# Kernel optimization log

Measured on AMD Instinct MI355X. Metric: run time of the kernel, lower is better.

Reference implementation:

```python
import math
import jax, jax.numpy as jnp
import numpy as np

G = 96       # grid side; N = G*G tokens, one token per grid cell
D = 512      # d_model
R = 2        # radius (Chebyshev)
LN_EPS = 1e-5

# 24 neighbor offsets in the (2R+1)^2 window, excluding (0,0) (self is excluded in the torch code)
_OFF = np.array([(dx, dy) for dx in range(-R, R + 1) for dy in range(-R, R + 1) if not (dx == 0 and dy == 0)], dtype=np.int32)


def _layer_norm(x, g, b):
    m = jnp.mean(x, axis=-1, keepdims=True)
    v = jnp.mean(jnp.square(x - m), axis=-1, keepdims=True)
    return (x - m) * jax.lax.rsqrt(v + LN_EPS) * g + b


def setup_inputs() -> dict:
    key = jax.random.key(0)
    ks = jax.random.split(key, 12)
    N = G * G
    x = jax.random.normal(ks[0], (N, D), jnp.float32)
    gx, gy = jnp.meshgrid(jnp.arange(G), jnp.arange(G), indexing='ij')
    grid = jnp.stack([gx.ravel(), gy.ravel()], axis=-1).astype(jnp.int32)  # [N,2], one token per cell

    def lin(k, din, dout):
        return jax.random.normal(k, (din, dout), jnp.float32) * (1.0 / math.sqrt(din))

    return {
        'x': x, 'grid': grid,
        'Wq': lin(ks[1], D, D), 'bq': jnp.zeros((D,), jnp.float32),
        'Wk': lin(ks[2], D, D), 'bk': jnp.zeros((D,), jnp.float32),
        'Wv': lin(ks[3], D, D), 'bv': jnp.zeros((D,), jnp.float32),
        'Wo': lin(ks[4], D, D), 'bo': jnp.zeros((D,), jnp.float32),
        'g1': jnp.ones((D,), jnp.float32), 'b1': jnp.zeros((D,), jnp.float32),
        'g2': jnp.ones((D,), jnp.float32), 'b2': jnp.zeros((D,), jnp.float32),
        'W1': lin(ks[5], D, 4 * D), 'bf1': jnp.zeros((4 * D,), jnp.float32),
        'W2': lin(ks[6], 4 * D, D), 'bf2': jnp.zeros((D,), jnp.float32),
    }


def reference(x, grid, Wq, bq, Wk, bk, Wv, bv, Wo, bo, g1, b1, g2, b2, W1, bf1, W2, bf2):
    # dropout is identity (eval mode)
    h = _layer_norm(x, g1, b1)
    q = h @ Wq + bq
    k = h @ Wk + bk
    v = h @ Wv + bv

    off = jnp.asarray(_OFF)                      # [K=24, 2]
    nx = grid[:, 0:1] + off[None, :, 0]          # [N, K]
    ny = grid[:, 1:2] + off[None, :, 1]
    valid = (nx >= 0) & (nx < G) & (ny >= 0) & (ny < G)
    idx = jnp.where(valid, nx * G + ny, 0)       # row-major cell -> token index

    k_nbr = k[idx]                               # [N, K, D]
    v_nbr = v[idx]                               # [N, K, D]
    scores = jnp.einsum('nd,nkd->nk', q, k_nbr) / math.sqrt(D)
    neg = jnp.finfo(scores.dtype).min
    scores = jnp.where(valid, scores, neg)
    attn = jax.nn.softmax(scores, axis=-1)       # every token has >=8 valid neighbors for G>R
    out = jnp.einsum('nk,nkd->nd', attn, v_nbr)  # [N, D]

    x = x + out @ Wo + bo
    h2 = _layer_norm(x, g2, b2)
    ffn = jax.nn.gelu(h2 @ W1 + bf1, approximate=False) @ W2 + bf2
    return x + ffn
```

## Files before the change

kernel.cpp:

```cpp
#include <hip/hip_runtime.h>

typedef unsigned short u16;
typedef unsigned int u32;
typedef __bf16 bf16x8 __attribute__((ext_vector_type(8)));
typedef float f32x4 __attribute__((ext_vector_type(4)));

#define GRID_G 96
#define DMODEL 512
#define NTOK (GRID_G * GRID_G)

__device__ __forceinline__ u16 f2bf(float f) {
  u32 u = __builtin_bit_cast(u32, f);
  u += 0x7fffu + ((u >> 16) & 1u);
  return (u16)(u >> 16);
}
__device__ __forceinline__ void unpack8(uint4 u, float* f) {
  f[0] = __builtin_bit_cast(float, u.x << 16);
  f[1] = __builtin_bit_cast(float, u.x & 0xffff0000u);
  f[2] = __builtin_bit_cast(float, u.y << 16);
  f[3] = __builtin_bit_cast(float, u.y & 0xffff0000u);
  f[4] = __builtin_bit_cast(float, u.z << 16);
  f[5] = __builtin_bit_cast(float, u.z & 0xffff0000u);
  f[6] = __builtin_bit_cast(float, u.w << 16);
  f[7] = __builtin_bit_cast(float, u.w & 0xffff0000u);
}
__device__ __forceinline__ float gelu_fast(float x) {
  float y = 0.7978845608f * (x + 0.044715f * x * x * x);
  float a = fabsf(y);
  float e = __expf(-2.0f * a);
  float th = (1.0f - e) / (1.0f + e);
  th = __builtin_copysignf(th, y);
  return 0.5f * x * (1.0f + th);
}

__global__ __launch_bounds__(256) void k_transpose_bf16(
    const float* __restrict__ src, u16* __restrict__ dst, int R, int C) {
  __shared__ float tile[32][33];
  int bx = blockIdx.x * 32, by = blockIdx.y * 32;
  int tx = threadIdx.x & 31, ty = threadIdx.x >> 5;
#pragma unroll
  for (int i = 0; i < 4; ++i) {
    int r = ty + i * 8;
    tile[r][tx] = src[(size_t)(by + r) * C + (bx + tx)];
  }
  __syncthreads();
#pragma unroll
  for (int i = 0; i < 4; ++i) {
    int c = ty + i * 8;
    dst[(size_t)(bx + c) * R + (by + tx)] = f2bf(tile[tx][c]);
  }
}

__global__ __launch_bounds__(256) void k_transpose4(
    const float* __restrict__ s0, const float* __restrict__ s1,
    const float* __restrict__ s2, const float* __restrict__ s3,
    u16* __restrict__ d0, u16* __restrict__ d1,
    u16* __restrict__ d2, u16* __restrict__ d3) {
  __shared__ float tile[32][33];
  const float* src = blockIdx.z == 0 ? s0 : blockIdx.z == 1 ? s1 : blockIdx.z == 2 ? s2 : s3;
  u16* dst = blockIdx.z == 0 ? d0 : blockIdx.z == 1 ? d1 : blockIdx.z == 2 ? d2 : d3;
  int bx = blockIdx.x * 32, by = blockIdx.y * 32;
  int tx = threadIdx.x & 31, ty = threadIdx.x >> 5;
#pragma unroll
  for (int i = 0; i < 4; ++i) {
    int r = ty + i * 8;
    tile[r][tx] = src[(size_t)(by + r) * 512 + (bx + tx)];
  }
  __syncthreads();
#pragma unroll
  for (int i = 0; i < 4; ++i) {
    int c = ty + i * 8;
    dst[(size_t)(bx + c) * 512 + (by + tx)] = f2bf(tile[tx][c]);
  }
}

__global__ __launch_bounds__(256) void k_concat3(
    const float* __restrict__ a, const float* __restrict__ b,
    const float* __restrict__ c, float* __restrict__ o) {
  int i = blockIdx.x * 256 + threadIdx.x;
  if (i < 512) o[i] = a[i];
  else if (i < 1024) o[i] = b[i - 512];
  else o[i] = c[i - 1024];
}

__global__ __launch_bounds__(256) void k_layernorm_bf16(
    const float* __restrict__ x, const float* __restrict__ g,
    const float* __restrict__ b, u16* __restrict__ out) {
  int tid = threadIdx.x, wid = tid >> 6, lane = tid & 63;
  int row = blockIdx.x * 4 + wid;
  const float* xr = x + (size_t)row * DMODEL;
  float4 v0 = *(const float4*)(xr + lane * 4);
  float4 v1 = *(const float4*)(xr + 256 + lane * 4);
  float s = v0.x + v0.y + v0.z + v0.w + v1.x + v1.y + v1.z + v1.w;
  float sq = v0.x * v0.x + v0.y * v0.y + v0.z * v0.z + v0.w * v0.w +
             v1.x * v1.x + v1.y * v1.y + v1.z * v1.z + v1.w * v1.w;
#pragma unroll
  for (int m = 1; m < 64; m <<= 1) {
    s += __shfl_xor(s, m);
    sq += __shfl_xor(sq, m);
  }
  float mean = s * (1.0f / DMODEL);
  float rstd = rsqrtf(sq * (1.0f / DMODEL) - mean * mean + 1e-5f);
  float4 ga = *(const float4*)(g + lane * 4);
  float4 gb = *(const float4*)(g + 256 + lane * 4);
  float4 ba = *(const float4*)(b + lane * 4);
  float4 bb = *(const float4*)(b + 256 + lane * 4);
  ushort4 o0, o1;
  o0.x = f2bf((v0.x - mean) * rstd * ga.x + ba.x);
  o0.y = f2bf((v0.y - mean) * rstd * ga.y + ba.y);
  o0.z = f2bf((v0.z - mean) * rstd * ga.z + ba.z);
  o0.w = f2bf((v0.w - mean) * rstd * ga.w + ba.w);
  o1.x = f2bf((v1.x - mean) * rstd * gb.x + bb.x);
  o1.y = f2bf((v1.y - mean) * rstd * gb.y + bb.y);
  o1.z = f2bf((v1.z - mean) * rstd * gb.z + bb.z);
  o1.w = f2bf((v1.w - mean) * rstd * gb.w + bb.w);
  u16* op = out + (size_t)row * DMODEL;
  *(ushort4*)(op + lane * 4) = o0;
  *(ushort4*)(op + 256 + lane * 4) = o1;
}

__global__ __launch_bounds__(256) void k_attn(
    const u16* __restrict__ q, const u16* __restrict__ kk,
    const u16* __restrict__ vv, const int* __restrict__ gpos,
    u16* __restrict__ out) {
  int tid = threadIdx.x, wid = tid >> 6, lane = tid & 63;
  int n = blockIdx.x * 4 + wid;
  int px = gpos[2 * n], py = gpos[2 * n + 1];
  float qf[8];
  unpack8(*(const uint4*)(q + (size_t)n * DMODEL + lane * 8), qf);
  float sc[24];
  int nid[24];
  bool ok[24];
#pragma unroll
  for (int j = 0; j < 24; ++j) {
    int jj = j < 12 ? j : j + 1;
    int dx = jj / 5 - 2, dy = jj % 5 - 2;
    int nx = px + dx, ny = py + dy;
    bool val = (nx >= 0) && (nx < GRID_G) && (ny >= 0) && (ny < GRID_G);
    int id = val ? nx * GRID_G + ny : 0;
    ok[j] = val;
    nid[j] = id;
    float kf[8];
    unpack8(*(const uint4*)(kk + (size_t)id * DMODEL + lane * 8), kf);
    float p = 0.f;
#pragma unroll
    for (int e = 0; e < 8; ++e) p += qf[e] * kf[e];
#pragma unroll
    for (int m = 1; m < 64; m <<= 1) p += __shfl_xor(p, m);
    sc[j] = p * 0.04419417382415922f;
  }
  float mx = -3.0e38f;
#pragma unroll
  for (int j = 0; j < 24; ++j)
    if (ok[j]) mx = fmaxf(mx, sc[j]);
  float wsum = 0.f, w[24];
#pragma unroll
  for (int j = 0; j < 24; ++j) {
    w[j] = ok[j] ? expf(sc[j] - mx) : 0.f;
    wsum += w[j];
  }
  float inv = 1.0f / wsum;
  float acc[8] = {0, 0, 0, 0, 0, 0, 0, 0};
#pragma unroll
  for (int j = 0; j < 24; ++j) {
    float vf[8];
    unpack8(*(const uint4*)(vv + (size_t)nid[j] * DMODEL + lane * 8), vf);
    float wj = w[j];
#pragma unroll
    for (int e = 0; e < 8; ++e) acc[e] += wj * vf[e];
  }
  uint4 o;
  o.x = (u32)f2bf(acc[0] * inv) | ((u32)f2bf(acc[1] * inv) << 16);
  o.y = (u32)f2bf(acc[2] * inv) | ((u32)f2bf(acc[3] * inv) << 16);
  o.z = (u32)f2bf(acc[4] * inv) | ((u32)f2bf(acc[5] * inv) << 16);
  o.w = (u32)f2bf(acc[6] * inv) | ((u32)f2bf(acc[7] * inv) << 16);
  *(uint4*)(out + (size_t)n * DMODEL + lane * 8) = o;
}

#define BARR { __builtin_amdgcn_s_barrier(); __builtin_amdgcn_sched_barrier(0); }
#define WAIT8 asm volatile("s_waitcnt vmcnt(8)" ::: "memory");
#define WAIT0 asm volatile("s_waitcnt vmcnt(0)" ::: "memory");

template <int EPI>
__global__ __launch_bounds__(256, 2) void k_gemm(
    const u16* __restrict__ A, const u16* __restrict__ Bt,
    const float* __restrict__ bias, const float* __restrict__ res,
    float* __restrict__ outF, u16* __restrict__ outB,
    int M, int N, int K, int tiles_n) {
  __shared__ u16 lds[32768];
  const int t = threadIdx.x, wid = t >> 6, lane = t & 63;
  const int nwg = gridDim.x, bid = blockIdx.x;
  const int l = ((bid & 7) * (nwg >> 3)) + (bid >> 3);
  const int bM = (l / tiles_n) * 128, bN = (l % tiles_n) * 128;
  const int wr = wid >> 1, wc = wid & 1, lr = lane & 15, lg = lane >> 4;

  const int rs = lane >> 3;
  const int cl = (lane & 7) ^ rs;
  const u16* gA[4];
  const u16* gB[4];
  int dstL[4];
#pragma unroll
  for (int j = 0; j < 4; ++j) {
    int r = wid * 32 + j * 8 + rs;
    gA[j] = A + (size_t)(bM + r) * K + cl * 8;
    gB[j] = Bt + (size_t)(bN + r) * K + cl * 8;
    dstL[j] = wid * 2048 + j * 512;
  }

#define STAGE(BUF, KOFF)                                                              \
  {                                                                                   \
    _Pragma("unroll") for (int j = 0; j < 4; ++j) {                                   \
      __builtin_amdgcn_global_load_lds(                                               \
          (const __attribute__((address_space(1))) void*)(gA[j] + (KOFF)),            \
          (__attribute__((address_space(3))) void*)(lds + (BUF)*16384 + dstL[j]),     \
          16, 0, 0);                                                                  \
      __builtin_amdgcn_global_load_lds(                                               \
          (const __attribute__((address_space(1))) void*)(gB[j] + (KOFF)),            \
          (__attribute__((address_space(3))) void*)(lds + (BUF)*16384 + 8192 + dstL[j]), \
          16, 0, 0);                                                                  \
    }                                                                                 \
  }

  const int offA0 = (wr * 64 + lr) * 64 + ((0 + lg) ^ (lr & 7)) * 8;
  const int offA1 = (wr * 64 + lr) * 64 + ((4 + lg) ^ (lr & 7)) * 8;
  const int offB0 = (wc * 64 + lr) * 64 + ((0 + lg) ^ (lr & 7)) * 8;
  const int offB1 = (wc * 64 + lr) * 64 + ((4 + lg) ^ (lr & 7)) * 8;

  f32x4 acc[4][4];
#pragma unroll
  for (int i = 0; i < 4; ++i)
#pragma unroll
    for (int j = 0; j < 4; ++j) acc[i][j] = (f32x4){0.f, 0.f, 0.f, 0.f};

#define COMPUTE(BUF)                                                                  \
  {                                                                                   \
    _Pragma("unroll") for (int ks = 0; ks < 2; ++ks) {                                \
      const int oa = (BUF)*16384 + (ks ? offA1 : offA0);                              \
      const int ob = (BUF)*16384 + 8192 + (ks ? offB1 : offB0);                       \
      bf16x8 af[4], bfr[4];                                                           \
      _Pragma("unroll") for (int mt = 0; mt < 4; ++mt)                                \
          af[mt] = __builtin_bit_cast(bf16x8, *(const uint4*)(lds + oa + mt * 1024)); \
      _Pragma("unroll") for (int nt = 0; nt < 4; ++nt)                                \
          bfr[nt] = __builtin_bit_cast(bf16x8, *(const uint4*)(lds + ob + nt * 1024));\
      _Pragma("unroll") for (int mt = 0; mt < 4; ++mt)                                \
          _Pragma("unroll") for (int nt = 0; nt < 4; ++nt)                            \
              acc[mt][nt] = __builtin_amdgcn_mfma_f32_16x16x32_bf16(                  \
                  af[mt], bfr[nt], acc[mt][nt], 0, 0, 0);                             \
    }                                                                                 \
  }

  const int nk = K >> 6;
  STAGE(0, 0);
  int koff = 64;
  for (int tt = 0; tt < nk; tt += 2) {
    if (tt + 1 < nk) { STAGE(1, koff); WAIT8 } else { WAIT0 }
    BARR;
    COMPUTE(0);
    BARR;
    if (tt + 2 < nk) { STAGE(0, koff + 64); WAIT8 } else { WAIT0 }
    BARR;
    COMPUTE(1);
    BARR;
    koff += 128;
  }
#undef STAGE
#undef COMPUTE

#pragma unroll
  for (int mt = 0; mt < 4; ++mt) {
#pragma unroll
    for (int nt = 0; nt < 4; ++nt) {
      int col = bN + wc * 64 + nt * 16 + lr;
      float bc = bias[col];
      int row0 = bM + wr * 64 + mt * 16 + lg * 4;
#pragma unroll
      for (int r = 0; r < 4; ++r) {
        float val = acc[mt][nt][r] + bc;
        if constexpr (EPI == 1) {
          size_t off = (size_t)(row0 + r) * N + col;
          outF[off] = res[off] + val;
        } else if constexpr (EPI == 2) {
          size_t off = (size_t)(row0 + r) * N + col;
          outB[off] = f2bf(gelu_fast(val));
        } else {
          int seg = col >> 9;
          size_t off = (size_t)seg * ((size_t)NTOK * DMODEL) +
                       (size_t)(row0 + r) * DMODEL + (col & 511);
          outB[off] = f2bf(val);
        }
      }
    }
  }
}

extern "C" void kernel_launch(void* const* d_in, const int* in_sizes, int n_in,
                              void* d_out, int out_size, void* d_ws, size_t ws_size,
                              hipStream_t stream) {
  const float* x = (const float*)d_in[0];
  const int* gpos = (const int*)d_in[1];
  const float* Wq = (const float*)d_in[2];
  const float* bq = (const float*)d_in[3];
  const float* Wk = (const float*)d_in[4];
  const float* bk = (const float*)d_in[5];
  const float* Wv = (const float*)d_in[6];
  const float* bv = (const float*)d_in[7];
  const float* Wo = (const float*)d_in[8];
  const float* bo = (const float*)d_in[9];
  const float* g1 = (const float*)d_in[10];
  const float* b1 = (const float*)d_in[11];
  const float* g2 = (const float*)d_in[12];
  const float* b2 = (const float*)d_in[13];
  const float* W1 = (const float*)d_in[14];
  const float* bf1 = (const float*)d_in[15];
  const float* W2 = (const float*)d_in[16];
  const float* bf2 = (const float*)d_in[17];
  float* out = (float*)d_out;
  char* ws = (char*)d_ws;

  constexpr size_t SZ_W512 = (size_t)512 * 512 * 2;
  constexpr size_t SZ_W2048 = (size_t)512 * 2048 * 2;
  constexpr size_t SZ_ACT = (size_t)NTOK * 512 * 2;

  u16* WQT = (u16*)(ws + 0);
  u16* WKT = (u16*)(ws + SZ_W512);
  u16* WVT = (u16*)(ws + 2 * SZ_W512);
  u16* WOT = (u16*)(ws + 3 * SZ_W512);
  u16* W1T = (u16*)(ws + 4 * SZ_W512);
  u16* W2T = (u16*)(ws + 4 * SZ_W512 + SZ_W2048);
  float* BCAT = (float*)(ws + 4 * SZ_W512 + 2 * SZ_W2048);
  char* actbase = ws + 4 * SZ_W512 + 2 * SZ_W2048 + 6144;
  u16* H = (u16*)(actbase);
  u16* Q = (u16*)(actbase + SZ_ACT);
  u16* KB = (u16*)(actbase + 2 * SZ_ACT);
  u16* VB = (u16*)(actbase + 3 * SZ_ACT);
  u16* H2 = (u16*)(actbase + 4 * SZ_ACT);
  u16* U = (u16*)(actbase);

  k_transpose4<<<dim3(16, 16, 4), 256, 0, stream>>>(Wq, Wk, Wv, Wo, WQT, WKT, WVT, WOT);
  k_transpose_bf16<<<dim3(64, 16), 256, 0, stream>>>(W1, W1T, 512, 2048);
  k_transpose_bf16<<<dim3(16, 64), 256, 0, stream>>>(W2, W2T, 2048, 512);
  k_concat3<<<6, 256, 0, stream>>>(bq, bk, bv, BCAT);

  k_layernorm_bf16<<<NTOK / 4, 256, 0, stream>>>(x, g1, b1, H);

  k_gemm<3><<<864, 256, 0, stream>>>(H, WQT, BCAT, nullptr, nullptr, Q, NTOK, 1536, 512, 12);

  k_attn<<<NTOK / 4, 256, 0, stream>>>(Q, KB, VB, gpos, H);

  k_gemm<1><<<288, 256, 0, stream>>>(H, WOT, bo, x, out, nullptr, NTOK, 512, 512, 4);

  k_layernorm_bf16<<<NTOK / 4, 256, 0, stream>>>(out, g2, b2, H2);

  k_gemm<2><<<1152, 256, 0, stream>>>(H2, W1T, bf1, nullptr, nullptr, U, NTOK, 2048, 512, 16);

  k_gemm<1><<<288, 256, 0, stream>>>(U, W2T, bf2, out, out, nullptr, NTOK, 512, 2048, 4);
}
```

Baseline: 164.9 us.

## Fuse prep kernels and add 256x256 pipelined GEMM for QKV and FFN1

Merges the weight transposes, bias concat and first layernorm into a single prep launch to cut launch overhead. Adds a new 512-thread GEMM with 256x256 tiles, direct global-to-LDS loads, XOR-swizzled LDS, double buffering interleaved with MFMA phases, and XCD-aware block remapping; it is used for the QKV and W1 projections. The rounding helper now uses the native bf16 conversion. The large tiles use 128KB of LDS and yield fewer blocks (216 and 288), which risks poor wave balance across CUs.

```diff
diff --git a/kernel.cpp b/kernel.cpp
--- a/kernel.cpp
+++ b/kernel.cpp
@@ -10,9 +10,7 @@
 #define NTOK (GRID_G * GRID_G)
 
 __device__ __forceinline__ u16 f2bf(float f) {
-  u32 u = __builtin_bit_cast(u32, f);
-  u += 0x7fffu + ((u >> 16) & 1u);
-  return (u16)(u >> 16);
+  return __builtin_bit_cast(u16, (__bf16)f);
 }
 __device__ __forceinline__ void unpack8(uint4 u, float* f) {
   f[0] = __builtin_bit_cast(float, u.x << 16);
@@ -33,54 +31,84 @@
   return 0.5f * x * (1.0f + th);
 }
 
-__global__ __launch_bounds__(256) void k_transpose_bf16(
-    const float* __restrict__ src, u16* __restrict__ dst, int R, int C) {
-  __shared__ float tile[32][33];
-  int bx = blockIdx.x * 32, by = blockIdx.y * 32;
+__device__ __forceinline__ void tr_tile(const float* __restrict__ src,
+                                        u16* __restrict__ dst, int R, int C,
+                                        int bx, int by, float (*tile)[33]) {
   int tx = threadIdx.x & 31, ty = threadIdx.x >> 5;
 #pragma unroll
   for (int i = 0; i < 4; ++i) {
     int r = ty + i * 8;
-    tile[r][tx] = src[(size_t)(by + r) * C + (bx + tx)];
+    tile[r][tx] = src[(size_t)(by * 32 + r) * C + (bx * 32 + tx)];
   }
   __syncthreads();
 #pragma unroll
   for (int i = 0; i < 4; ++i) {
     int c = ty + i * 8;
-    dst[(size_t)(bx + c) * R + (by + tx)] = f2bf(tile[tx][c]);
-  }
-}
-
-__global__ __launch_bounds__(256) void k_transpose4(
-    const float* __restrict__ s0, const float* __restrict__ s1,
-    const float* __restrict__ s2, const float* __restrict__ s3,
-    u16* __restrict__ d0, u16* __restrict__ d1,
-    u16* __restrict__ d2, u16* __restrict__ d3) {
+    dst[(size_t)(bx * 32 + c) * R + (by * 32 + tx)] = f2bf(tile[tx][c]);
+  }
+}
+
+__global__ __launch_bounds__(256) void k_prep(
+    const float* __restrict__ Wq, const float* __restrict__ Wk,
+    const float* __restrict__ Wv, const float* __restrict__ Wo,
+    const float* __restrict__ W1, const float* __restrict__ W2,
+    const float* __restrict__ bq, const float* __restrict__ bk,
+    const float* __restrict__ bv, const float* __restrict__ x,
+    const float* __restrict__ g1, const float* __restrict__ b1,
+    u16* __restrict__ WQT, u16* __restrict__ WKT, u16* __restrict__ WVT,
+    u16* __restrict__ WOT, u16* __restrict__ W1T, u16* __restrict__ W2T,
+    float* __restrict__ BCAT, u16* __restrict__ H) {
   __shared__ float tile[32][33];
-  const float* src = blockIdx.z == 0 ? s0 : blockIdx.z == 1 ? s1 : blockIdx.z == 2 ? s2 : s3;
-  u16* dst = blockIdx.z == 0 ? d0 : blockIdx.z == 1 ? d1 : blockIdx.z == 2 ? d2 : d3;
-  int bx = blockIdx.x * 32, by = blockIdx.y * 32;
-  int tx = threadIdx.x & 31, ty = threadIdx.x >> 5;
-#pragma unroll
-  for (int i = 0; i < 4; ++i) {
-    int r = ty + i * 8;
-    tile[r][tx] = src[(size_t)(by + r) * 512 + (bx + tx)];
-  }
-  __syncthreads();
-#pragma unroll
-  for (int i = 0; i < 4; ++i) {
-    int c = ty + i * 8;
-    dst[(size_t)(bx + c) * 512 + (by + tx)] = f2bf(tile[tx][c]);
-  }
-}
-
-__global__ __launch_bounds__(256) void k_concat3(
-    const float* __restrict__ a, const float* __restrict__ b,
-    const float* __restrict__ c, float* __restrict__ o) {
-  int i = blockIdx.x * 256 + threadIdx.x;
-  if (i < 512) o[i] = a[i];
-  else if (i < 1024) o[i] = b[i - 512];
-  else o[i] = c[i - 1024];
+  const int b = blockIdx.x;
+  if (b < 1024) {
+    int z = b >> 8, sub = b & 255;
+    const float* s = z == 0 ? Wq : z == 1 ? Wk : z == 2 ? Wv : Wo;
+    u16* d = z == 0 ? WQT : z == 1 ? WKT : z == 2 ? WVT : WOT;
+    tr_tile(s, d, 512, 512, sub & 15, sub >> 4, tile);
+  } else if (b < 2048) {
+    int idx = b - 1024;
+    tr_tile(W1, W1T, 512, 2048, idx & 63, idx >> 6, tile);
+  } else if (b < 3072) {
+    int idx = b - 2048;
+    tr_tile(W2, W2T, 2048, 512, idx & 15, idx >> 4, tile);
+  } else if (b < 3078) {
+    int i = (b - 3072) * 256 + threadIdx.x;
+    if (i < 512) BCAT[i] = bq[i];
+    else if (i < 1024) BCAT[i] = bk[i - 512];
+    else if (i < 1536) BCAT[i] = bv[i - 1024];
+  } else {
+    int tid = threadIdx.x, wid = tid >> 6, lane = tid & 63;
+    int row = (b - 3078) * 4 + wid;
+    const float* xr = x + (size_t)row * DMODEL;
+    float4 v0 = *(const float4*)(xr + lane * 4);
+    float4 v1 = *(const float4*)(xr + 256 + lane * 4);
+    float s = v0.x + v0.y + v0.z + v0.w + v1.x + v1.y + v1.z + v1.w;
+    float sq = v0.x * v0.x + v0.y * v0.y + v0.z * v0.z + v0.w * v0.w +
+               v1.x * v1.x + v1.y * v1.y + v1.z * v1.z + v1.w * v1.w;
+#pragma unroll
+    for (int m = 1; m < 64; m <<= 1) {
+      s += __shfl_xor(s, m);
+      sq += __shfl_xor(sq, m);
+    }
+    float mean = s * (1.0f / DMODEL);
+    float rstd = rsqrtf(sq * (1.0f / DMODEL) - mean * mean + 1e-5f);
+    float4 ga = *(const float4*)(g1 + lane * 4);
+    float4 gb = *(const float4*)(g1 + 256 + lane * 4);
+    float4 ba = *(const float4*)(b1 + lane * 4);
+    float4 bb = *(const float4*)(b1 + 256 + lane * 4);
+    ushort4 o0, o1;
+    o0.x = f2bf((v0.x - mean) * rstd * ga.x + ba.x);
+    o0.y = f2bf((v0.y - mean) * rstd * ga.y + ba.y);
+    o0.z = f2bf((v0.z - mean) * rstd * ga.z + ba.z);
+    o0.w = f2bf((v0.w - mean) * rstd * ga.w + ba.w);
+    o1.x = f2bf((v1.x - mean) * rstd * gb.x + bb.x);
+    o1.y = f2bf((v1.y - mean) * rstd * gb.y + bb.y);
+    o1.z = f2bf((v1.z - mean) * rstd * gb.z + bb.z);
+    o1.w = f2bf((v1.w - mean) * rstd * gb.w + bb.w);
+    u16* op = H + (size_t)row * DMODEL;
+    *(ushort4*)(op + lane * 4) = o0;
+    *(ushort4*)(op + 256 + lane * 4) = o1;
+  }
 }
 
 __global__ __launch_bounds__(256) void k_layernorm_bf16(
@@ -276,18 +304,129 @@
 #pragma unroll
       for (int r = 0; r < 4; ++r) {
         float val = acc[mt][nt][r] + bc;
+        size_t off = (size_t)(row0 + r) * N + col;
         if constexpr (EPI == 1) {
-          size_t off = (size_t)(row0 + r) * N + col;
           outF[off] = res[off] + val;
-        } else if constexpr (EPI == 2) {
-          size_t off = (size_t)(row0 + r) * N + col;
-          outB[off] = f2bf(gelu_fast(val));
         } else {
-          int seg = col >> 9;
-          size_t off = (size_t)seg * ((size_t)NTOK * DMODEL) +
-                       (size_t)(row0 + r) * DMODEL + (col & 511);
           outB[off] = f2bf(val);
         }
+      }
+    }
+  }
+}
+
+#define BARR2 { __builtin_amdgcn_sched_barrier(0); __builtin_amdgcn_s_barrier(); __builtin_amdgcn_sched_barrier(0); }
+#define WAITV0 asm volatile("s_waitcnt vmcnt(0)" ::: "memory");
+#define WAITV2 asm volatile("s_waitcnt vmcnt(2)" ::: "memory");
+#define WAITV4 asm volatile("s_waitcnt vmcnt(4)" ::: "memory");
+
+template <int EPI, int KDIM>
+__global__ __launch_bounds__(512, 2) void k_gemm_big(
+    const u16* __restrict__ A, const u16* __restrict__ Bt,
+    const float* __restrict__ bias, u16* __restrict__ outB,
+    int N, int tiles_n) {
+  __shared__ u16 lds[65536];
+  const int t = threadIdx.x, wid = t >> 6, lane = t & 63;
+  const int wr = wid >> 2, wc = wid & 3;
+  const int lr = lane & 15, lg = lane >> 4;
+  const int nwg = gridDim.x, bid = blockIdx.x;
+  const int qq = nwg >> 3, rr = nwg & 7;
+  const int xcd = bid & 7, seq = bid >> 3;
+  const int l = (xcd < rr ? xcd * (qq + 1) : rr * (qq + 1) + (xcd - rr) * qq) + seq;
+  const int bM = (l / tiles_n) * 256, bN = (l % tiles_n) * 256;
+
+  const int srow = wid * 8 + (lane >> 3);
+  const int cl = (lane & 7) ^ (lane >> 3);
+  const u16* pA = A + (size_t)(bM + srow) * KDIM + cl * 8;
+  const u16* pB = Bt + (size_t)(bN + srow) * KDIM + cl * 8;
+  const int dbase = wid * 512;
+
+#define STG(C, BOFF, PTR, H, KT)                                                       \
+  { _Pragma("unroll") for (int j = 0; j < 2; ++j)                                      \
+      __builtin_amdgcn_global_load_lds(                                                \
+        (const __attribute__((address_space(1))) void*)((PTR) + (size_t)((H)*128 + j*64) * KDIM + (KT)), \
+        (__attribute__((address_space(3))) void*)(lds + (C) + (BOFF) + (H)*8192 + dbase + j*4096), \
+        16, 0, 0); }
+
+  const int swz0 = ((0 + lg) ^ (lr & 7)) * 8;
+  const int swz1 = ((4 + lg) ^ (lr & 7)) * 8;
+
+  f32x4 acc[4][8];
+#pragma unroll
+  for (int q = 0; q < 4; ++q)
+#pragma unroll
+    for (int rf = 0; rf < 8; ++rf) acc[q][rf] = (f32x4){0.f, 0.f, 0.f, 0.f};
+
+  bf16x8 a[8][2], b0, b1;
+
+#define READ_A(C)                                                                      \
+  { _Pragma("unroll") for (int rf = 0; rf < 8; ++rf) {                                 \
+      const u16* ab = lds + (C) + (wr * 128 + rf * 16 + lr) * 64;                      \
+      a[rf][0] = __builtin_bit_cast(bf16x8, *(const uint4*)(ab + swz0));               \
+      a[rf][1] = __builtin_bit_cast(bf16x8, *(const uint4*)(ab + swz1)); } }
+
+#define READ_B(C, Q)                                                                   \
+  { const u16* bb = lds + (C) + 16384 + ((Q)*64 + wc * 16 + lr) * 64;                  \
+    b0 = __builtin_bit_cast(bf16x8, *(const uint4*)(bb + swz0));                       \
+    b1 = __builtin_bit_cast(bf16x8, *(const uint4*)(bb + swz1)); }
+
+#define MFMA_PH(Q)                                                                     \
+  { __builtin_amdgcn_s_setprio(1);                                                     \
+    _Pragma("unroll") for (int rf = 0; rf < 8; ++rf) {                                 \
+      acc[Q][rf] = __builtin_amdgcn_mfma_f32_16x16x32_bf16(a[rf][0], b0, acc[Q][rf], 0, 0, 0); \
+      acc[Q][rf] = __builtin_amdgcn_mfma_f32_16x16x32_bf16(a[rf][1], b1, acc[Q][rf], 0, 0, 0); } \
+    __builtin_amdgcn_s_setprio(0); }
+
+  STG(0, 0, pA, 0, 0); STG(0, 0, pA, 1, 0);
+  STG(0, 16384, pB, 0, 0); STG(0, 16384, pB, 1, 0);
+  WAITV0;
+  BARR2;
+
+  constexpr int nk = KDIM >> 6;
+  for (int tt = 0; tt < nk; ++tt) {
+    const int c = (tt & 1) << 15;
+    const int cn = c ^ 32768;
+    const int kn = (tt + 1) << 6;
+    const bool pre = tt + 1 < nk;
+    READ_A(c); READ_B(c, 0);
+    if (pre) STG(cn, 0, pA, 0, kn);
+    BARR2; MFMA_PH(0); BARR2;
+    READ_B(c, 1);
+    if (pre) { STG(cn, 0, pA, 1, kn); WAITV4 } else { WAITV0 }
+    BARR2; MFMA_PH(1); BARR2;
+    READ_B(c, 2);
+    if (pre) STG(cn, 16384, pB, 0, kn);
+    BARR2; MFMA_PH(2); BARR2;
+    READ_B(c, 3);
+    if (pre) { STG(cn, 16384, pB, 1, kn); WAITV2 }
+    BARR2; MFMA_PH(3); BARR2;
+  }
+#undef STG
+#undef READ_A
+#undef READ_B
+#undef MFMA_PH
+
+#pragma unroll
+  for (int q = 0; q < 4; ++q) {
+    const int colb = bN + q * 64 + wc * 16 + lr;
+    const float bc = bias[colb];
+    if constexpr (EPI == 2) {
+#pragma unroll
+      for (int rf = 0; rf < 8; ++rf) {
+        const int row0 = bM + wr * 128 + rf * 16 + lg * 4;
+#pragma unroll
+        for (int r = 0; r < 4; ++r)
+          outB[(size_t)(row0 + r) * N + colb] = f2bf(gelu_fast(acc[q][rf][r] + bc));
+      }
+    } else {
+      const int seg = colb >> 9;
+      u16* base = outB + (size_t)seg * ((size_t)NTOK * DMODEL) + (colb & 511);
+#pragma unroll
+      for (int rf = 0; rf < 8; ++rf) {
+        const int row0 = bM + wr * 128 + rf * 16 + lg * 4;
+#pragma unroll
+        for (int r = 0; r < 4; ++r)
+          base[(size_t)(row0 + r) * DMODEL] = f2bf(acc[q][rf][r] + bc);
       }
     }
   }
@@ -336,14 +475,10 @@
   u16* H2 = (u16*)(actbase + 4 * SZ_ACT);
   u16* U = (u16*)(actbase);
 
-  k_transpose4<<<dim3(16, 16, 4), 256, 0, stream>>>(Wq, Wk, Wv, Wo, WQT, WKT, WVT, WOT);
-  k_transpose_bf16<<<dim3(64, 16), 256, 0, stream>>>(W1, W1T, 512, 2048);
-  k_transpose_bf16<<<dim3(16, 64), 256, 0, stream>>>(W2, W2T, 2048, 512);
-  k_concat3<<<6, 256, 0, stream>>>(bq, bk, bv, BCAT);
-
-  k_layernorm_bf16<<<NTOK / 4, 256, 0, stream>>>(x, g1, b1, H);
-
-  k_gemm<3><<<864, 256, 0, stream>>>(H, WQT, BCAT, nullptr, nullptr, Q, NTOK, 1536, 512, 12);
+  k_prep<<<5382, 256, 0, stream>>>(Wq, Wk, Wv, Wo, W1, W2, bq, bk, bv, x, g1, b1,
+                                   WQT, WKT, WVT, WOT, W1T, W2T, BCAT, H);
+
+  k_gemm_big<3, 512><<<216, 512, 0, stream>>>(H, WQT, BCAT, Q, 1536, 6);
 
   k_attn<<<NTOK / 4, 256, 0, stream>>>(Q, KB, VB, gpos, H);
 
@@ -351,7 +486,7 @@
 
   k_layernorm_bf16<<<NTOK / 4, 256, 0, stream>>>(out, g2, b2, H2);
 
-  k_gemm<2><<<1152, 256, 0, stream>>>(H2, W1T, bf1, nullptr, nullptr, U, NTOK, 2048, 512, 16);
+  k_gemm_big<2, 512><<<288, 512, 0, stream>>>(H2, W1T, bf1, U, 2048, 8);
 
   k_gemm<1><<<288, 256, 0, stream>>>(U, W2T, bf2, out, out, nullptr, NTOK, 512, 2048, 4);
 }
```

New measurement: 170.8 us. 1.04x slower.
